# Performance work log

Measured on AMD Instinct MI355X. Metric: run time of the kernel, lower is better.

Reference implementation:

```python
import jax, jax.numpy as jnp
import numpy as np

QMAX = 7.0   # int4 symmetric, narrow range [-7, 7] per weight; acts use [-8, 7]
QMIN = -8.0

def _ste_quant(v, scale, qmin, qmax):
    """Symmetric per-tensor fake-quant with straight-through estimator."""
    s = jax.lax.stop_gradient(scale)
    q = jnp.clip(jnp.round(v / s), qmin, qmax) * s
    return v + jax.lax.stop_gradient(q - v)


def setup_inputs() -> dict:
    key = jax.random.key(0)
    k1, k2, k3 = jax.random.split(key, 3)
    d_model, vocab = 1024, 50257
    x = jax.random.normal(k1, (2, 1024, d_model), jnp.float32)
    W = jax.random.normal(k2, (vocab, d_model), jnp.float32) * 0.02
    b = jax.random.normal(k3, (vocab,), jnp.float32) * 0.01
    return {"x": x, "W": W, "b": b}


def reference(x, W, b):
    # Activation quant: 4-bit signed, per-tensor scale from max-abs stats
    sx = jnp.max(jnp.abs(x)) / QMAX
    xq = _ste_quant(x, sx, QMIN, QMAX)
    # Weight quant: 4-bit signed per-tensor
    sw = jnp.max(jnp.abs(W)) / QMAX
    wq = _ste_quant(W, sw, QMIN, QMAX)
    # Int32 bias: quantized at the accumulator scale sx*sw (range huge -> round only)
    sb = jax.lax.stop_gradient(sx * sw)
    bq = b + jax.lax.stop_gradient(jnp.round(b / sb) * sb - b)
    # Quantized GEMM with int32-style accumulation, expressed as dequantized matmul
    logits = jnp.einsum('bsd,vd->bsv', xq, wq) + bq  # [B, S, vocab]
    return jax.nn.log_softmax(logits, axis=-1)
```

## Files before the change

### kernel.cpp

```cpp
#include <hip/hip_runtime.h>
#include <hip/hip_bf16.h>

#define N_VOCAB 50257
#define NB      393
#define N_PAD   50304
#define D_K     1024
#define M_ROWS  2048
#define GEMM_BLOCKS (NB * 16)
#define PER_XCD     (GEMM_BLOCKS/8)

typedef __attribute__((ext_vector_type(4))) int i32x4;

__device__ inline void async_copy16(const void* g, void* l) {
  auto* gp = (const __attribute__((address_space(1))) unsigned int*)g;
  auto* lp = (__attribute__((address_space(3))) unsigned int*)l;
  __builtin_amdgcn_global_load_lds(gp, lp, 16, 0, 0);
}

__device__ inline signed char qint(float v, float s) {
  float q = fminf(fmaxf(rintf(v / s), -8.f), 7.f);
  return (signed char)(int)q;
}

__global__ void absmax2_kernel(const float4* __restrict__ x, int nx4,
                               const float4* __restrict__ Wp, int nw4,
                               unsigned* __restrict__ amax) {
  const bool isx = blockIdx.x < 512;
  const float4* p = isx ? x : Wp;
  const int n4 = isx ? nx4 : nw4;
  const int b0 = isx ? blockIdx.x : blockIdx.x - 512;
  const int nb = isx ? 512 : (gridDim.x - 512);
  float m = 0.f;
  for (int i = b0 * blockDim.x + threadIdx.x; i < n4; i += nb * blockDim.x) {
    float4 v = p[i];
    m = fmaxf(m, fmaxf(fmaxf(fabsf(v.x), fabsf(v.y)),
                       fmaxf(fabsf(v.z), fabsf(v.w))));
  }
#pragma unroll
  for (int off = 32; off; off >>= 1) m = fmaxf(m, __shfl_xor(m, off));
  __shared__ float red[4];
  int tid = threadIdx.x;
  if ((tid & 63) == 0) red[tid >> 6] = m;
  __syncthreads();
  if (tid == 0) {
    m = fmaxf(fmaxf(red[0], red[1]), fmaxf(red[2], red[3]));
    atomicMax(&amax[isx ? 0 : 1], __float_as_uint(m));
  }
}

__global__ void quant_kernel(const float4* __restrict__ x,
                             const float4* __restrict__ Wp,
                             const float* __restrict__ b,
                             char4* __restrict__ qx, char4* __restrict__ qw,
                             float* __restrict__ bq,
                             const unsigned* __restrict__ amax) {
  const int bid = blockIdx.x;
  const int tid = threadIdx.x;
  const int nw4 = (N_VOCAB * D_K) / 4;
  if (bid < 2048) {
    int i = bid * 256 + tid;
    float s = __uint_as_float(amax[0]) * (1.0f / 7.0f);
    float4 v = x[i];
    char4 q;
    q.x = qint(v.x, s); q.y = qint(v.y, s);
    q.z = qint(v.z, s); q.w = qint(v.w, s);
    qx[i] = q;
  } else if (bid < 2048 + 50304) {
    int i = (bid - 2048) * 256 + tid;
    char4 q = {0, 0, 0, 0};
    if (i < nw4) {
      float s = __uint_as_float(amax[1]) * (1.0f / 7.0f);
      float4 v = Wp[i];
      q.x = qint(v.x, s); q.y = qint(v.y, s);
      q.z = qint(v.z, s); q.w = qint(v.w, s);
    }
    qw[i] = q;
  } else {
    int i = (bid - (2048 + 50304)) * 256 + tid;
    if (i < N_PAD) {
      float v = 0.f;
      if (i < N_VOCAB) {
        float sb = (__uint_as_float(amax[0]) * (1.0f / 7.0f)) *
                   (__uint_as_float(amax[1]) * (1.0f / 7.0f));
        v = rintf(b[i] / sb) * sb;
      }
      bq[i] = v;
    }
  }
}

__global__ __launch_bounds__(256, 4) void gemm_kernel(
    const signed char* __restrict__ qx,
    const signed char* __restrict__ qw,
    const float* __restrict__ bq,
    const unsigned* __restrict__ amax,
    float* __restrict__ outp,
    float* __restrict__ pmax,
    float* __restrict__ psum)
{
  constexpr int BK = 64;
  constexpr int NT = D_K / BK;
  __shared__ __align__(16) signed char sA[2][128 * BK];
  __shared__ __align__(16) signed char sB[3][128 * BK];

  const int tid = threadIdx.x;
  const int l = tid & 63;
  const int w = tid >> 6;
  const int wr = w >> 1, wc = w & 1;

  const int bid = blockIdx.x;
  const int vb = (bid & 7) * PER_XCD + (bid >> 3);
  const int nb = vb >> 4;
  const int m0 = (vb & 15) * 128;
  const int n0 = nb * 128;

  const float sx = __uint_as_float(amax[0]) * (1.0f / 7.0f);
  const float sw = __uint_as_float(amax[1]) * (1.0f / 7.0f);
  const float scale = sx * sw;

  i32x4 acc[4][4] = {};

  const int srow = l >> 2;
  const int scol = ((l & 3) ^ ((l >> 3) & 3)) * 16;

  auto stageA = [&](int buf, int kt) {
    int k0 = kt * BK;
#pragma unroll
    for (int i = 0; i < 2; ++i) {
      int c = w * 2 + i;
      int row = c * 16 + srow;
      async_copy16(qx + (size_t)(m0 + row) * D_K + k0 + scol,
                   &sA[buf][c * 1024]);
    }
  };
  auto stageB = [&](int buf, int kt) {
    int k0 = kt * BK;
#pragma unroll
    for (int i = 0; i < 2; ++i) {
      int c = w * 2 + i;
      int row = c * 16 + srow;
      async_copy16(qw + (size_t)(n0 + row) * D_K + k0 + scol,
                   &sB[buf][c * 1024]);
    }
  };

  stageA(0, 0);
  stageB(0, 0);
  stageB(1, 1);
  asm volatile("s_waitcnt vmcnt(2)" ::: "memory");
  __builtin_amdgcn_s_barrier();
  __builtin_amdgcn_sched_barrier(0);

#pragma unroll
  for (int kt = 0; kt < NT; ++kt) {
    const int ca = kt & 1;
    const int cb = kt % 3;

    i32x4 af[4], bfr[4];
#pragma unroll
    for (int mi = 0; mi < 4; ++mi) {
      int row = wr * 64 + mi * 16 + (l & 15);
      int kb = ((l >> 4) ^ ((row >> 1) & 3)) * 16;
      af[mi] = *(const i32x4*)&sA[ca][row * BK + kb];
    }
#pragma unroll
    for (int ni = 0; ni < 4; ++ni) {
      int row = wc * 64 + ni * 16 + (l & 15);
      int kb = ((l >> 4) ^ ((row >> 1) & 3)) * 16;
      bfr[ni] = *(const i32x4*)&sB[cb][row * BK + kb];
    }

    if (kt + 1 < NT) stageA(ca ^ 1, kt + 1);
    if (kt + 2 < NT) stageB((kt + 2) % 3, kt + 2);

    __builtin_amdgcn_s_setprio(1);
#pragma unroll
    for (int mi = 0; mi < 4; ++mi)
#pragma unroll
      for (int ni = 0; ni < 4; ++ni)
        acc[mi][ni] = __builtin_amdgcn_mfma_i32_16x16x64_i8(
            af[mi], bfr[ni], acc[mi][ni], 0, 0, 0);
    __builtin_amdgcn_s_setprio(0);
    __builtin_amdgcn_sched_barrier(0);

    if (kt + 1 < NT) {
      if (kt + 2 < NT)
        asm volatile("s_waitcnt vmcnt(2)" ::: "memory");
      else
        asm volatile("s_waitcnt vmcnt(0)" ::: "memory");
      __builtin_amdgcn_s_barrier();
      __builtin_amdgcn_sched_barrier(0);
    }
  }

  bool valid[4];
  float bb[4];
#pragma unroll
  for (int ni = 0; ni < 4; ++ni) {
    int col = n0 + wc * 64 + ni * 16 + (l & 15);
    valid[ni] = (col < N_VOCAB);
    bb[ni] = valid[ni] ? bq[col] : 0.f;
  }
  float lg[4][4][4];
#pragma unroll
  for (int mi = 0; mi < 4; ++mi)
#pragma unroll
    for (int ni = 0; ni < 4; ++ni)
#pragma unroll
      for (int r = 0; r < 4; ++r)
        lg[mi][ni][r] = (float)acc[mi][ni][r] * scale + bb[ni];

  __syncthreads();
  float* redMax = (float*)&sB[0][0];
  float* redSum = redMax + 256;

  float rmax[4][4];
#pragma unroll
  for (int mi = 0; mi < 4; ++mi)
#pragma unroll
    for (int r = 0; r < 4; ++r) {
      float mval = -3.4e38f;
#pragma unroll
      for (int ni = 0; ni < 4; ++ni)
        if (valid[ni]) mval = fmaxf(mval, lg[mi][ni][r]);
#pragma unroll
      for (int off = 1; off < 16; off <<= 1)
        mval = fmaxf(mval, __shfl_xor(mval, off));
      rmax[mi][r] = mval;
      if ((l & 15) == 0)
        redMax[(wr * 64 + mi * 16 + (l >> 4) * 4 + r) * 2 + wc] = mval;
    }
  __syncthreads();

#pragma unroll
  for (int mi = 0; mi < 4; ++mi)
#pragma unroll
    for (int r = 0; r < 4; ++r) {
      int rl = wr * 64 + mi * 16 + (l >> 4) * 4 + r;
      float gmax = fmaxf(redMax[rl * 2 + 0], redMax[rl * 2 + 1]);
      float s = 0.f;
#pragma unroll
      for (int ni = 0; ni < 4; ++ni)
        if (valid[ni]) s += __expf(lg[mi][ni][r] - gmax);
#pragma unroll
      for (int off = 1; off < 16; off <<= 1)
        s += __shfl_xor(s, off);
      if ((l & 15) == 0) redSum[rl * 2 + wc] = s;
      rmax[mi][r] = gmax;
    }
  __syncthreads();

  if (wc == 0 && (l & 15) == 0) {
#pragma unroll
    for (int mi = 0; mi < 4; ++mi)
#pragma unroll
      for (int r = 0; r < 4; ++r) {
        int rl = wr * 64 + mi * 16 + (l >> 4) * 4 + r;
        int rowg = m0 + rl;
        pmax[(size_t)rowg * NB + nb] = rmax[mi][r];
        psum[(size_t)rowg * NB + nb] = redSum[rl * 2 + 0] + redSum[rl * 2 + 1];
      }
  }

#pragma unroll
  for (int mi = 0; mi < 4; ++mi)
#pragma unroll
    for (int r = 0; r < 4; ++r) {
      int rowg = m0 + wr * 64 + mi * 16 + (l >> 4) * 4 + r;
      size_t rb = (size_t)rowg * N_VOCAB;
#pragma unroll
      for (int ni = 0; ni < 4; ++ni) {
        if (valid[ni]) {
          int col = n0 + wc * 64 + ni * 16 + (l & 15);
          outp[rb + col] = lg[mi][ni][r];
        }
      }
    }
}

__global__ __launch_bounds__(256) void logz_sub_kernel(
    const float* __restrict__ pmax, const float* __restrict__ psum,
    float* __restrict__ out) {
  const int row = blockIdx.x;
  const float* pm = pmax + (size_t)row * NB;
  const float* ps = psum + (size_t)row * NB;
  const int tid = threadIdx.x;
  __shared__ float red[9];

  float m = -3.4e38f;
  for (int i = tid; i < NB; i += 256) m = fmaxf(m, pm[i]);
#pragma unroll
  for (int off = 32; off; off >>= 1) m = fmaxf(m, __shfl_xor(m, off));
  if ((tid & 63) == 0) red[tid >> 6] = m;
  __syncthreads();
  m = fmaxf(fmaxf(red[0], red[1]), fmaxf(red[2], red[3]));

  float s = 0.f;
  for (int i = tid; i < NB; i += 256) s += ps[i] * __expf(pm[i] - m);
#pragma unroll
  for (int off = 32; off; off >>= 1) s += __shfl_xor(s, off);
  if ((tid & 63) == 0) red[4 + (tid >> 6)] = s;
  __syncthreads();
  if (tid == 0) {
    s = red[4] + red[5] + red[6] + red[7];
    red[8] = m + __logf(s);
  }
  __syncthreads();
  const float lz = red[8];

  const size_t base = (size_t)row * N_VOCAB;
  const int a = (4 - (row & 3)) & 3;
  if (tid < a) out[base + tid] -= lz;
  const int n4 = (N_VOCAB - a) >> 2;
  float4* p = (float4*)(out + base + a);
  for (int i = tid; i < n4; i += 256) {
    float4 v = p[i];
    v.x -= lz; v.y -= lz; v.z -= lz; v.w -= lz;
    p[i] = v;
  }
  const int done = a + n4 * 4;
  if (tid < N_VOCAB - done) out[base + done + tid] -= lz;
}

extern "C" void kernel_launch(void* const* d_in, const int* in_sizes, int n_in,
                              void* d_out, int out_size, void* d_ws,
                              size_t ws_size, hipStream_t stream) {
  const float* x = (const float*)d_in[0];
  const float* W = (const float*)d_in[1];
  const float* b = (const float*)d_in[2];
  float* out = (float*)d_out;

  char* ws = (char*)d_ws;
  unsigned* amax = (unsigned*)ws;
  float* bq = (float*)(ws + 4096);
  float* pmax = (float*)(ws + (2ull << 20));
  float* psum = (float*)(ws + (6ull << 20));
  signed char* qx = (signed char*)(ws + (10ull << 20));
  signed char* qw = (signed char*)(ws + (14ull << 20));

  hipMemsetAsync(amax, 0, 8, stream);

  const int nx4 = (M_ROWS * D_K) / 4;
  const int nw4 = (N_VOCAB * D_K) / 4;

  absmax2_kernel<<<2560, 256, 0, stream>>>((const float4*)x, nx4,
                                           (const float4*)W, nw4, amax);

  quant_kernel<<<2048 + 50304 + 197, 256, 0, stream>>>(
      (const float4*)x, (const float4*)W, b, (char4*)qx, (char4*)qw, bq, amax);

  gemm_kernel<<<GEMM_BLOCKS, 256, 0, stream>>>(qx, qw, bq, amax, out, pmax,
                                               psum);

  logz_sub_kernel<<<M_ROWS, 256, 0, stream>>>(pmax, psum, out);
}
```

Before: 553.3 us.

## Widen quant stores, deepen B pipeline, recompute logits, split logz subtract

The quantize kernel now packs eight int8 values into one 64-bit store per thread and reads two float4s, halving the block count. The GEMM gains a fourth B shared-memory buffer so B tiles prefetch three stages ahead, and the epilogue recomputes logits from the accumulators instead of holding a 64-float array, which lowers register pressure. The absmax grid is widened for the weight pass, and the logz subtract kernel splits each row across four blocks for more parallelism. The risks are the larger LDS footprint lowering occupancy, and each of the four logz blocks recomputing the row reduction.

Result: slower. 617.6 us (+11.6%).

```diff
diff --git a/kernel.cpp b/kernel.cpp
--- a/kernel.cpp
+++ b/kernel.cpp
@@ -17,14 +17,14 @@
   __builtin_amdgcn_global_load_lds(gp, lp, 16, 0, 0);
 }
 
-__device__ inline signed char qint(float v, float s) {
+__device__ inline unsigned long long q8(float v, float s) {
   float q = fminf(fmaxf(rintf(v / s), -8.f), 7.f);
-  return (signed char)(int)q;
-}
-
-__global__ void absmax2_kernel(const float4* __restrict__ x, int nx4,
-                               const float4* __restrict__ Wp, int nw4,
-                               unsigned* __restrict__ amax) {
+  return (unsigned long long)(unsigned char)(signed char)(int)q;
+}
+
+__global__ __launch_bounds__(256) void absmax2_kernel(
+    const float4* __restrict__ x, int nx4, const float4* __restrict__ Wp,
+    int nw4, unsigned* __restrict__ amax) {
   const bool isx = blockIdx.x < 512;
   const float4* p = isx ? x : Wp;
   const int n4 = isx ? nx4 : nw4;
@@ -48,35 +48,35 @@
   }
 }
 
-__global__ void quant_kernel(const float4* __restrict__ x,
-                             const float4* __restrict__ Wp,
-                             const float* __restrict__ b,
-                             char4* __restrict__ qx, char4* __restrict__ qw,
-                             float* __restrict__ bq,
-                             const unsigned* __restrict__ amax) {
+#define XB8  1024
+#define WB8  25152
+__global__ __launch_bounds__(256) void quant_kernel(
+    const float4* __restrict__ x, const float4* __restrict__ Wp,
+    const float* __restrict__ b, unsigned long long* __restrict__ qx,
+    unsigned long long* __restrict__ qw, float* __restrict__ bq,
+    const unsigned* __restrict__ amax) {
   const int bid = blockIdx.x;
   const int tid = threadIdx.x;
-  const int nw4 = (N_VOCAB * D_K) / 4;
-  if (bid < 2048) {
+  if (bid < XB8) {
     int i = bid * 256 + tid;
     float s = __uint_as_float(amax[0]) * (1.0f / 7.0f);
-    float4 v = x[i];
-    char4 q;
-    q.x = qint(v.x, s); q.y = qint(v.y, s);
-    q.z = qint(v.z, s); q.w = qint(v.w, s);
-    qx[i] = q;
-  } else if (bid < 2048 + 50304) {
-    int i = (bid - 2048) * 256 + tid;
-    char4 q = {0, 0, 0, 0};
-    if (i < nw4) {
+    float4 a = x[2 * i], c = x[2 * i + 1];
+    qx[i] = q8(a.x, s) | q8(a.y, s) << 8 | q8(a.z, s) << 16 |
+            q8(a.w, s) << 24 | q8(c.x, s) << 32 | q8(c.y, s) << 40 |
+            q8(c.z, s) << 48 | q8(c.w, s) << 56;
+  } else if (bid < XB8 + WB8) {
+    int i = (bid - XB8) * 256 + tid;
+    unsigned long long v = 0ull;
+    if (i < N_VOCAB * (D_K / 8)) {
       float s = __uint_as_float(amax[1]) * (1.0f / 7.0f);
-      float4 v = Wp[i];
-      q.x = qint(v.x, s); q.y = qint(v.y, s);
-      q.z = qint(v.z, s); q.w = qint(v.w, s);
-    }
-    qw[i] = q;
+      float4 a = Wp[2 * i], c = Wp[2 * i + 1];
+      v = q8(a.x, s) | q8(a.y, s) << 8 | q8(a.z, s) << 16 | q8(a.w, s) << 24 |
+          q8(c.x, s) << 32 | q8(c.y, s) << 40 | q8(c.z, s) << 48 |
+          q8(c.w, s) << 56;
+    }
+    qw[i] = v;
   } else {
-    int i = (bid - (2048 + 50304)) * 256 + tid;
+    int i = (bid - (XB8 + WB8)) * 256 + tid;
     if (i < N_PAD) {
       float v = 0.f;
       if (i < N_VOCAB) {
@@ -101,7 +101,7 @@
   constexpr int BK = 64;
   constexpr int NT = D_K / BK;
   __shared__ __align__(16) signed char sA[2][128 * BK];
-  __shared__ __align__(16) signed char sB[3][128 * BK];
+  __shared__ __align__(16) signed char sB[4][128 * BK];
 
   const int tid = threadIdx.x;
   const int l = tid & 63;
@@ -147,14 +147,15 @@
   stageA(0, 0);
   stageB(0, 0);
   stageB(1, 1);
-  asm volatile("s_waitcnt vmcnt(2)" ::: "memory");
+  stageB(2, 2);
+  asm volatile("s_waitcnt vmcnt(4)" ::: "memory");
   __builtin_amdgcn_s_barrier();
   __builtin_amdgcn_sched_barrier(0);
 
 #pragma unroll
   for (int kt = 0; kt < NT; ++kt) {
     const int ca = kt & 1;
-    const int cb = kt % 3;
+    const int cb = kt & 3;
 
     i32x4 af[4], bfr[4];
 #pragma unroll
@@ -171,7 +172,7 @@
     }
 
     if (kt + 1 < NT) stageA(ca ^ 1, kt + 1);
-    if (kt + 2 < NT) stageB((kt + 2) % 3, kt + 2);
+    if (kt + 3 < NT) stageB((kt + 3) & 3, kt + 3);
 
     __builtin_amdgcn_s_setprio(1);
 #pragma unroll
@@ -184,7 +185,7 @@
     __builtin_amdgcn_sched_barrier(0);
 
     if (kt + 1 < NT) {
-      if (kt + 2 < NT)
+      if (kt + 3 < NT)
         asm volatile("s_waitcnt vmcnt(2)" ::: "memory");
       else
         asm volatile("s_waitcnt vmcnt(0)" ::: "memory");
@@ -201,20 +202,13 @@
     valid[ni] = (col < N_VOCAB);
     bb[ni] = valid[ni] ? bq[col] : 0.f;
   }
-  float lg[4][4][4];
-#pragma unroll
-  for (int mi = 0; mi < 4; ++mi)
-#pragma unroll
-    for (int ni = 0; ni < 4; ++ni)
-#pragma unroll
-      for (int r = 0; r < 4; ++r)
-        lg[mi][ni][r] = (float)acc[mi][ni][r] * scale + bb[ni];
+#define LGT(mi, ni, r) ((float)acc[mi][ni][r] * scale + bb[ni])
 
   __syncthreads();
   float* redMax = (float*)&sB[0][0];
   float* redSum = redMax + 256;
 
-  float rmax[4][4];
+  float gm[4][4];
 #pragma unroll
   for (int mi = 0; mi < 4; ++mi)
 #pragma unroll
@@ -222,11 +216,10 @@
       float mval = -3.4e38f;
 #pragma unroll
       for (int ni = 0; ni < 4; ++ni)
-        if (valid[ni]) mval = fmaxf(mval, lg[mi][ni][r]);
+        if (valid[ni]) mval = fmaxf(mval, LGT(mi, ni, r));
 #pragma unroll
       for (int off = 1; off < 16; off <<= 1)
         mval = fmaxf(mval, __shfl_xor(mval, off));
-      rmax[mi][r] = mval;
       if ((l & 15) == 0)
         redMax[(wr * 64 + mi * 16 + (l >> 4) * 4 + r) * 2 + wc] = mval;
     }
@@ -241,12 +234,12 @@
       float s = 0.f;
 #pragma unroll
       for (int ni = 0; ni < 4; ++ni)
-        if (valid[ni]) s += __expf(lg[mi][ni][r] - gmax);
+        if (valid[ni]) s += __expf(LGT(mi, ni, r) - gmax);
 #pragma unroll
       for (int off = 1; off < 16; off <<= 1)
         s += __shfl_xor(s, off);
       if ((l & 15) == 0) redSum[rl * 2 + wc] = s;
-      rmax[mi][r] = gmax;
+      gm[mi][r] = gmax;
     }
   __syncthreads();
 
@@ -257,7 +250,7 @@
       for (int r = 0; r < 4; ++r) {
         int rl = wr * 64 + mi * 16 + (l >> 4) * 4 + r;
         int rowg = m0 + rl;
-        pmax[(size_t)rowg * NB + nb] = rmax[mi][r];
+        pmax[(size_t)rowg * NB + nb] = gm[mi][r];
         psum[(size_t)rowg * NB + nb] = redSum[rl * 2 + 0] + redSum[rl * 2 + 1];
       }
   }
@@ -272,16 +265,18 @@
       for (int ni = 0; ni < 4; ++ni) {
         if (valid[ni]) {
           int col = n0 + wc * 64 + ni * 16 + (l & 15);
-          outp[rb + col] = lg[mi][ni][r];
+          outp[rb + col] = LGT(mi, ni, r);
         }
       }
     }
+#undef LGT
 }
 
 __global__ __launch_bounds__(256) void logz_sub_kernel(
     const float* __restrict__ pmax, const float* __restrict__ psum,
     float* __restrict__ out) {
-  const int row = blockIdx.x;
+  const int row = blockIdx.x >> 2;
+  const int part = blockIdx.x & 3;
   const float* pm = pmax + (size_t)row * NB;
   const float* ps = psum + (size_t)row * NB;
   const int tid = threadIdx.x;
@@ -310,16 +305,22 @@
 
   const size_t base = (size_t)row * N_VOCAB;
   const int a = (4 - (row & 3)) & 3;
-  if (tid < a) out[base + tid] -= lz;
   const int n4 = (N_VOCAB - a) >> 2;
+  const int p4 = (n4 + 3) >> 2;
+  const int i0 = part * p4;
+  const int i1 = min(n4, i0 + p4);
   float4* p = (float4*)(out + base + a);
-  for (int i = tid; i < n4; i += 256) {
+  for (int i = i0 + tid; i < i1; i += 256) {
     float4 v = p[i];
     v.x -= lz; v.y -= lz; v.z -= lz; v.w -= lz;
     p[i] = v;
   }
-  const int done = a + n4 * 4;
-  if (tid < N_VOCAB - done) out[base + done + tid] -= lz;
+  if (part == 0) {
+    if (tid < a) out[base + tid] -= lz;
+  } else if (part == 3) {
+    const int done = a + n4 * 4;
+    if (tid < N_VOCAB - done) out[base + done + tid] -= lz;
+  }
 }
 
 extern "C" void kernel_launch(void* const* d_in, const int* in_sizes, int n_in,
@@ -343,14 +344,15 @@
   const int nx4 = (M_ROWS * D_K) / 4;
   const int nw4 = (N_VOCAB * D_K) / 4;
 
-  absmax2_kernel<<<2560, 256, 0, stream>>>((const float4*)x, nx4,
-                                           (const float4*)W, nw4, amax);
-
-  quant_kernel<<<2048 + 50304 + 197, 256, 0, stream>>>(
-      (const float4*)x, (const float4*)W, b, (char4*)qx, (char4*)qw, bq, amax);
+  absmax2_kernel<<<512 + 4096, 256, 0, stream>>>((const float4*)x, nx4,
+                                                 (const float4*)W, nw4, amax);
+
+  quant_kernel<<<XB8 + WB8 + 197, 256, 0, stream>>>(
+      (const float4*)x, (const float4*)W, b, (unsigned long long*)qx,
+      (unsigned long long*)qw, bq, amax);
 
   gemm_kernel<<<GEMM_BLOCKS, 256, 0, stream>>>(qx, qw, bq, amax, out, pmax,
                                                psum);
 
-  logz_sub_kernel<<<M_ROWS, 256, 0, stream>>>(pmax, psum, out);
-}
+  logz_sub_kernel<<<M_ROWS * 4, 256, 0, stream>>>(pmax, psum, out);
+}
```
